# Kernel tuning notes

Measured on AMD Instinct MI355X. Metric: run time of the kernel, lower is better.

Reference implementation:

```python
import jax, jax.numpy as jnp
import numpy as np

D_K = 64
SCALE = D_K ** (-0.5)
B, H, S = 2, 16, 2048


def setup_inputs() -> dict:
    key = jax.random.key(0)
    kq, kk, kv = jax.random.split(key, 3)
    q = jax.random.normal(kq, (B, H, S, D_K), dtype=jnp.float32)
    k = jax.random.normal(kk, (B, H, S, D_K), dtype=jnp.float32)
    v = jax.random.normal(kv, (B, H, S, D_K), dtype=jnp.float32)
    # causal mask: True means masked (matches torch masked_fill semantics)
    mask = jnp.triu(jnp.ones((S, S), dtype=bool), k=1)[None, None]  # [1,1,S,S]
    return {"q": q, "k": k, "v": v, "mask": mask}


def reference(q, k, v, mask) -> jnp.ndarray:
    # scores = q @ k^T  -> [B,H,S,S]
    scores = jnp.einsum("bhqd,bhkd->bhqk", q, k)
    # masked_fill(mask, -inf), then scale (as written in the source),
    # then softmax over the key axis. -inf * scale stays -inf.
    scores = jnp.where(mask, -jnp.inf, scores)
    attn = jax.nn.softmax(SCALE * scores, axis=-1)
    return jnp.einsum("bhqk,bhkd->bhqd", attn, v)
```

## Files before the change

kernel.cpp:

```cpp
#include <hip/hip_runtime.h>
#include <hip/hip_bf16.h>
#include <math.h>


constexpr int S  = 2048;
constexpr int D  = 64;
constexpr int BH = 32;
constexpr float SCALE = 0.125f;
constexpr float LOG2E = 1.4426950408889634f;
constexpr float QPRE  = SCALE * LOG2E;
constexpr int PSTR = 72;

typedef __attribute__((ext_vector_type(8))) short bf16x8;
typedef __attribute__((ext_vector_type(4))) short bf16x4;
typedef __attribute__((ext_vector_type(4))) float f32x4;

#if __has_builtin(__builtin_amdgcn_mfma_f32_16x16x16bf16_1k)
#define HAS_MFMA_1K 1
#else
#define HAS_MFMA_1K 0
#endif

#if __has_builtin(__builtin_amdgcn_exp2f)
#define EXP2F(x) __builtin_amdgcn_exp2f(x)
#else
#define EXP2F(x) exp2f(x)
#endif

__device__ __forceinline__ short f2bf(float x) {
    union { __hip_bfloat16 b; short s; } u; u.b = __float2bfloat16(x); return u.s;
}

__device__ __forceinline__ void gload_lds16(const void* g, void* lds) {
    __builtin_amdgcn_global_load_lds(
        (const __attribute__((address_space(1))) unsigned int*)g,
        (__attribute__((address_space(3))) unsigned int*)lds, 16, 0, 0);
}

__global__ __launch_bounds__(256) void preconv_25993142075924(
    const float* __restrict__ Kg, const float* __restrict__ Vg,
    short* __restrict__ Kb, short* __restrict__ VT)
{
    const int kt = blockIdx.x, bh = blockIdx.y, tid = threadIdx.x;
    __shared__ float lt[64 * 65];
    const float* kp = Kg + (size_t)bh * S * D;
    const float* vp = Vg + (size_t)bh * S * D;
    short* kb = Kb + (size_t)bh * S * D;
    short* vt = VT + (size_t)bh * D * S;
    #pragma unroll
    for (int e = 0; e < 4; ++e) {
        int idx = (tid + e * 256) * 4;
        int r = idx >> 6, c = idx & 63;
        f32x4 k4 = *(const f32x4*)(kp + (size_t)(kt * 64 + r) * D + c);
        bf16x4 kb4;
        kb4[0] = f2bf(k4[0]); kb4[1] = f2bf(k4[1]);
        kb4[2] = f2bf(k4[2]); kb4[3] = f2bf(k4[3]);
        *(bf16x4*)(kb + (size_t)(kt * 64 + r) * D + c) = kb4;
        f32x4 v4 = *(const f32x4*)(vp + (size_t)(kt * 64 + r) * D + c);
        lt[(c + 0) * 65 + r] = v4[0];
        lt[(c + 1) * 65 + r] = v4[1];
        lt[(c + 2) * 65 + r] = v4[2];
        lt[(c + 3) * 65 + r] = v4[3];
    }
    __syncthreads();
    #pragma unroll
    for (int e = 0; e < 2; ++e) {
        int tt = tid + e * 256;
        int d  = tt >> 3;
        int j0 = (tt & 7) * 8;
        bf16x8 o;
        #pragma unroll
        for (int jj = 0; jj < 8; ++jj)
            o[jj] = f2bf(lt[d * 65 + j0 + jj]);
        *(bf16x8*)(vt + (size_t)d * S + kt * 64 + j0) = o;
    }
}

__global__ __launch_bounds__(256, 3) void attn_fwd_v8_25993142075924(
    const float* __restrict__ Qg, const short* __restrict__ Kb,
    const short* __restrict__ VT, float* __restrict__ Og)
{
    const int bh  = blockIdx.x;
    const int qb  = 31 - (int)blockIdx.y;
    const int tid = threadIdx.x;
    const int wv  = tid >> 6;
    const int ln  = tid & 63;
    const int c16 = ln & 15;
    const int qd  = ln >> 4;

    const int q0  = qb * 64 + wv * 16;
    const int nkt = qb + 1;

    __shared__ __align__(16) short lk[2][64 * 64];
    __shared__ __align__(16) short lv[2][64 * 64];
#if !HAS_MFMA_1K
    __shared__ __align__(16) short lp[4 * 16 * PSTR];
    short* lpw = lp + wv * 16 * PSTR;
#endif

    const float* qp = Qg + (size_t)bh * S * D;
    const short* kp = Kb + (size_t)bh * S * D;
    const short* vp = VT + (size_t)bh * D * S;
    float*       op = Og + (size_t)bh * S * D;

    const int srow0 = wv * 16 + (ln >> 3);
    const int sgrp0 = (ln & 7) ^ (srow0 & 7);
    const int srow1 = srow0 + 8;
    const int sgrp1 = (ln & 7) ^ (srow1 & 7);

    bf16x8 qf[2];
    {
        const float* src = qp + (size_t)(q0 + c16) * D + qd * 8;
        #pragma unroll
        for (int khf = 0; khf < 2; ++khf) {
            f32x4 a = *(const f32x4*)(src + khf * 32);
            f32x4 b = *(const f32x4*)(src + khf * 32 + 4);
            bf16x8 f;
            f[0] = f2bf(a[0] * QPRE); f[1] = f2bf(a[1] * QPRE);
            f[2] = f2bf(a[2] * QPRE); f[3] = f2bf(a[3] * QPRE);
            f[4] = f2bf(b[0] * QPRE); f[5] = f2bf(b[1] * QPRE);
            f[6] = f2bf(b[2] * QPRE); f[7] = f2bf(b[3] * QPRE);
            qf[khf] = f;
        }
    }

    f32x4 oacc[4] = {{0,0,0,0},{0,0,0,0},{0,0,0,0},{0,0,0,0}};
    float lsum = 0.f;

    gload_lds16(kp + (size_t)srow0 * D + sgrp0 * 8, &lk[0][(wv * 16 + 0) * 64]);
    gload_lds16(vp + (size_t)srow0 * S + sgrp0 * 8, &lv[0][(wv * 16 + 0) * 64]);
    gload_lds16(kp + (size_t)srow1 * D + sgrp1 * 8, &lk[0][(wv * 16 + 8) * 64]);
    gload_lds16(vp + (size_t)srow1 * S + sgrp1 * 8, &lv[0][(wv * 16 + 8) * 64]);
    __syncthreads();

    for (int kt = 0; kt < nkt; ++kt) {
        const int cur = kt & 1;
        if (kt + 1 < nkt) {
            const int nxt = cur ^ 1;
            const size_t kb0 = (size_t)(kt + 1) * 64;
            gload_lds16(kp + (kb0 + srow0) * D + sgrp0 * 8, &lk[nxt][(wv * 16 + 0) * 64]);
            gload_lds16(vp + (size_t)srow0 * S + kb0 + sgrp0 * 8, &lv[nxt][(wv * 16 + 0) * 64]);
            gload_lds16(kp + (kb0 + srow1) * D + sgrp1 * 8, &lk[nxt][(wv * 16 + 8) * 64]);
            gload_lds16(vp + (size_t)srow1 * S + kb0 + sgrp1 * 8, &lv[nxt][(wv * 16 + 8) * 64]);
        }

#if HAS_MFMA_1K
        bf16x4 vf[4][4];
        #pragma unroll
        for (int dt = 0; dt < 4; ++dt) {
            const int row = dt * 16 + c16;
            #pragma unroll
            for (int nt = 0; nt < 4; ++nt) {
                const int gl = nt * 2 + (qd >> 1);
                const int gp = gl ^ (c16 & 7);
                vf[dt][nt] = *(const bf16x4*)&lv[cur][row * 64 + gp * 8 + (qd & 1) * 4];
            }
        }
#endif

        float t[4][4];
        #pragma unroll
        for (int nt = 0; nt < 4; ++nt) {
            const int row = nt * 16 + c16;
            f32x4 acc = {0,0,0,0};
            #pragma unroll
            for (int khf = 0; khf < 2; ++khf) {
                const int g = (khf * 4 + qd) ^ (row & 7);
                bf16x8 kf = *(const bf16x8*)&lk[cur][row * 64 + g * 8];
                acc = __builtin_amdgcn_mfma_f32_16x16x32_bf16(kf, qf[khf], acc, 0, 0, 0);
            }
            t[nt][0] = acc[0]; t[nt][1] = acc[1]; t[nt][2] = acc[2]; t[nt][3] = acc[3];
        }

        if (kt == qb) {
            #pragma unroll
            for (int nt = 0; nt < 4; ++nt) {
                #pragma unroll
                for (int r = 0; r < 4; ++r) {
                    int key = kt * 64 + nt * 16 + qd * 4 + r;
                    if (key > q0 + c16) t[nt][r] = -INFINITY;
                }
            }
        }

        float pval[4][4];
        #pragma unroll
        for (int nt = 0; nt < 4; ++nt)
            #pragma unroll
            for (int r = 0; r < 4; ++r) {
                float pv = EXP2F(t[nt][r]);
                pval[nt][r] = pv;
                lsum += pv;
            }

#if HAS_MFMA_1K
        #pragma unroll
        for (int nt = 0; nt < 4; ++nt) {
            bf16x4 pf;
            pf[0] = f2bf(pval[nt][0]); pf[1] = f2bf(pval[nt][1]);
            pf[2] = f2bf(pval[nt][2]); pf[3] = f2bf(pval[nt][3]);
            #pragma unroll
            for (int dt = 0; dt < 4; ++dt)
                oacc[dt] = __builtin_amdgcn_mfma_f32_16x16x16bf16_1k(
                    vf[dt][nt], pf, oacc[dt], 0, 0, 0);
        }
#else
        #pragma unroll
        for (int nt = 0; nt < 4; ++nt)
            #pragma unroll
            for (int r = 0; r < 4; ++r)
                lpw[c16 * PSTR + nt * 16 + qd * 4 + r] = f2bf(pval[nt][r]);
        bf16x8 pf2[2];
        #pragma unroll
        for (int khf = 0; khf < 2; ++khf)
            pf2[khf] = *(const bf16x8*)&lpw[c16 * PSTR + khf * 32 + qd * 8];
        #pragma unroll
        for (int dt = 0; dt < 4; ++dt) {
            const int row = dt * 16 + c16;
            #pragma unroll
            for (int khf = 0; khf < 2; ++khf) {
                const int g = (khf * 4 + qd) ^ (row & 7);
                bf16x8 vf8 = *(const bf16x8*)&lv[cur][row * 64 + g * 8];
                oacc[dt] = __builtin_amdgcn_mfma_f32_16x16x32_bf16(vf8, pf2[khf], oacc[dt], 0, 0, 0);
            }
        }
#endif

        __syncthreads();
    }

    float s = lsum;
    s += __shfl_xor(s, 16);
    s += __shfl_xor(s, 32);
    const float inv = 1.0f / s;
    float* dst = op + (size_t)(q0 + c16) * D;
    #pragma unroll
    for (int dt = 0; dt < 4; ++dt) {
        f32x4 o;
        o[0] = oacc[dt][0] * inv; o[1] = oacc[dt][1] * inv;
        o[2] = oacc[dt][2] * inv; o[3] = oacc[dt][3] * inv;
        *(f32x4*)(dst + dt * 16 + qd * 4) = o;
    }
}

__global__ __launch_bounds__(256) void attn_fwd_v1_25993142075924(
    const float* __restrict__ Qg, const float* __restrict__ Kg,
    const float* __restrict__ Vg, float* __restrict__ Og)
{
    constexpr int KSTR = 72;
    constexpr int BQ = 64, BK = 64;
    const int qt  = blockIdx.x;
    const int bh  = blockIdx.y;
    const int tid = threadIdx.x;
    const int wv  = tid >> 6;
    const int ln  = tid & 63;
    const int c16 = ln & 15;
    const int qd  = ln >> 4;

    __shared__ __align__(16) __hip_bfloat16 lk [BK][KSTR];
    __shared__ __align__(16) __hip_bfloat16 lvt[D ][KSTR];
    __shared__ __align__(16) __hip_bfloat16 lp [4][16][KSTR];

    const size_t hoff = (size_t)bh * S * D;
    const float* qp = Qg + hoff;
    const float* kp = Kg + hoff;
    const float* vp = Vg + hoff;
    float*       op = Og + hoff;
    const int q0 = qt * BQ;

    bf16x8 qf[2];
    {
        const float* src = qp + (size_t)(q0 + wv*16 + c16) * D + qd*8;
        #pragma unroll
        for (int kh = 0; kh < 2; ++kh) {
            f32x4 a = *(const f32x4*)(src + kh*32);
            f32x4 b = *(const f32x4*)(src + kh*32 + 4);
            bf16x8 f;
            f[0]=f2bf(a[0]*QPRE); f[1]=f2bf(a[1]*QPRE); f[2]=f2bf(a[2]*QPRE); f[3]=f2bf(a[3]*QPRE);
            f[4]=f2bf(b[0]*QPRE); f[5]=f2bf(b[1]*QPRE); f[6]=f2bf(b[2]*QPRE); f[7]=f2bf(b[3]*QPRE);
            qf[kh] = f;
        }
    }

    f32x4 oacc[4] = {{0,0,0,0},{0,0,0,0},{0,0,0,0},{0,0,0,0}};
    float mrun[4] = {-INFINITY,-INFINITY,-INFINITY,-INFINITY};
    float lrun[4] = {0.f,0.f,0.f,0.f};

    const int nkt = qt + 1;
    for (int kt = 0; kt < nkt; ++kt) {
        __syncthreads();
        #pragma unroll
        for (int e = 0; e < 4; ++e) {
            int idx = (tid + e*256) * 4;
            int row = idx >> 6, col = idx & 63;
            f32x4 k4 = *(const f32x4*)(kp + (size_t)(kt*BK + row)*D + col);
            bf16x4 kb;
            kb[0]=f2bf(k4[0]); kb[1]=f2bf(k4[1]); kb[2]=f2bf(k4[2]); kb[3]=f2bf(k4[3]);
            *(bf16x4*)&lk[row][col] = kb;
            f32x4 v4 = *(const f32x4*)(vp + (size_t)(kt*BK + row)*D + col);
            lvt[col+0][row] = __float2bfloat16(v4[0]);
            lvt[col+1][row] = __float2bfloat16(v4[1]);
            lvt[col+2][row] = __float2bfloat16(v4[2]);
            lvt[col+3][row] = __float2bfloat16(v4[3]);
        }
        __syncthreads();

        float t[4][4];
        #pragma unroll
        for (int nt = 0; nt < 4; ++nt) {
            f32x4 acc = {0,0,0,0};
            #pragma unroll
            for (int kh = 0; kh < 2; ++kh) {
                bf16x8 kf = *(const bf16x8*)&lk[nt*16 + c16][kh*32 + qd*8];
                acc = __builtin_amdgcn_mfma_f32_16x16x32_bf16(qf[kh], kf, acc, 0, 0, 0);
            }
            #pragma unroll
            for (int r = 0; r < 4; ++r) t[nt][r] = acc[r];
        }
        if (kt == nkt - 1) {
            #pragma unroll
            for (int nt = 0; nt < 4; ++nt) {
                int j = kt*BK + nt*16 + c16;
                #pragma unroll
                for (int r = 0; r < 4; ++r)
                    if (j > q0 + wv*16 + qd*4 + r) t[nt][r] = -INFINITY;
            }
        }

        float pval[4][4];
        #pragma unroll
        for (int r = 0; r < 4; ++r) {
            float tm = fmaxf(fmaxf(t[0][r], t[1][r]), fmaxf(t[2][r], t[3][r]));
            tm = fmaxf(tm, __shfl_xor(tm, 1));
            tm = fmaxf(tm, __shfl_xor(tm, 2));
            tm = fmaxf(tm, __shfl_xor(tm, 4));
            tm = fmaxf(tm, __shfl_xor(tm, 8));
            float mnew  = fmaxf(mrun[r], tm);
            float alpha = exp2f(mrun[r] - mnew);
            mrun[r] = mnew;
            float rs = 0.f;
            #pragma unroll
            for (int nt = 0; nt < 4; ++nt) {
                float pv = exp2f(t[nt][r] - mnew);
                pval[nt][r] = pv;
                rs += pv;
            }
            rs += __shfl_xor(rs, 1);
            rs += __shfl_xor(rs, 2);
            rs += __shfl_xor(rs, 4);
            rs += __shfl_xor(rs, 8);
            lrun[r] = lrun[r] * alpha + rs;
            #pragma unroll
            for (int dt = 0; dt < 4; ++dt) oacc[dt][r] *= alpha;
        }

        #pragma unroll
        for (int nt = 0; nt < 4; ++nt)
            #pragma unroll
            for (int r = 0; r < 4; ++r)
                lp[wv][qd*4 + r][nt*16 + c16] = __float2bfloat16(pval[nt][r]);
        bf16x8 pf[2];
        #pragma unroll
        for (int kh = 0; kh < 2; ++kh)
            pf[kh] = *(const bf16x8*)&lp[wv][c16][kh*32 + qd*8];

        #pragma unroll
        for (int dt = 0; dt < 4; ++dt) {
            #pragma unroll
            for (int kh = 0; kh < 2; ++kh) {
                bf16x8 vf = *(const bf16x8*)&lvt[dt*16 + c16][kh*32 + qd*8];
                oacc[dt] = __builtin_amdgcn_mfma_f32_16x16x32_bf16(pf[kh], vf, oacc[dt], 0, 0, 0);
            }
        }
    }

    #pragma unroll
    for (int r = 0; r < 4; ++r) {
        float inv = 1.0f / lrun[r];
        float* dst = op + (size_t)(q0 + wv*16 + qd*4 + r) * D;
        #pragma unroll
        for (int dt = 0; dt < 4; ++dt)
            dst[dt*16 + c16] = oacc[dt][r] * inv;
    }
}

extern "C" void kernel_launch(void* const* d_in, const int* in_sizes, int n_in,
                              void* d_out, int out_size, void* d_ws, size_t ws_size,
                              hipStream_t stream) {
    const float* q = (const float*)d_in[0];
    const float* k = (const float*)d_in[1];
    const float* v = (const float*)d_in[2];
    float* out = (float*)d_out;
    const size_t elems = (size_t)BH * S * D;
    const size_t need  = 2 * elems * sizeof(short);
    if (ws_size >= need) {
        short* Kb = (short*)d_ws;
        short* VT = Kb + elems;
        preconv_25993142075924<<<dim3(S / 64, BH), 256, 0, stream>>>(k, v, Kb, VT);
        attn_fwd_v8_25993142075924<<<dim3(BH, 32), 256, 0, stream>>>(q, Kb, VT, out);
    } else {
        attn_fwd_v1_25993142075924<<<dim3(S / 64, BH), 256, 0, stream>>>(q, k, v, out);
    }
}
```

Baseline: 137.1 us.

## Process 128 query rows per block, reusing K/V tiles across two query sub-tiles

Each block now covers 128 query rows instead of 64, and each wave handles two 16-row query sub-tiles. Every K and V tile loaded into LDS therefore feeds twice the MFMA work, which halves the global-to-LDS traffic per query. Waves skip compute on tiles that lie fully above their causal diagonal. The launch bound drops to 2 blocks per SM, the grid halves to 16 q-blocks per head ordered in a zig-zag to balance causal work, and register pressure rises. Some waves idle on diagonal tiles.

```diff
diff --git a/kernel.cpp b/kernel.cpp
--- a/kernel.cpp
+++ b/kernel.cpp
@@ -76,20 +76,22 @@
     }
 }
 
-__global__ __launch_bounds__(256, 3) void attn_fwd_v8_25993142075924(
+__global__ __launch_bounds__(256, 2) void attn_fwd_v9_25993142075924(
     const float* __restrict__ Qg, const short* __restrict__ Kb,
     const short* __restrict__ VT, float* __restrict__ Og)
 {
     const int bh  = blockIdx.x;
-    const int qb  = 31 - (int)blockIdx.y;
+    const int yy  = blockIdx.y;
+    const int qb  = (yy < 8) ? (15 - yy) : (yy - 8);
     const int tid = threadIdx.x;
     const int wv  = tid >> 6;
     const int ln  = tid & 63;
     const int c16 = ln & 15;
     const int qd  = ln >> 4;
 
-    const int q0  = qb * 64 + wv * 16;
-    const int nkt = qb + 1;
+    const int w0    = qb * 128 + wv * 32;
+    const int nkt   = 2 * qb + 2;
+    const int mask0 = w0 >> 6;
 
     __shared__ __align__(16) short lk[2][64 * 64];
     __shared__ __align__(16) short lv[2][64 * 64];
@@ -108,9 +110,10 @@
     const int srow1 = srow0 + 8;
     const int sgrp1 = (ln & 7) ^ (srow1 & 7);
 
-    bf16x8 qf[2];
-    {
-        const float* src = qp + (size_t)(q0 + c16) * D + qd * 8;
+    bf16x8 qf[2][2];
+    #pragma unroll
+    for (int sp = 0; sp < 2; ++sp) {
+        const float* src = qp + (size_t)(w0 + sp * 16 + c16) * D + qd * 8;
         #pragma unroll
         for (int khf = 0; khf < 2; ++khf) {
             f32x4 a = *(const f32x4*)(src + khf * 32);
@@ -120,12 +123,13 @@
             f[2] = f2bf(a[2] * QPRE); f[3] = f2bf(a[3] * QPRE);
             f[4] = f2bf(b[0] * QPRE); f[5] = f2bf(b[1] * QPRE);
             f[6] = f2bf(b[2] * QPRE); f[7] = f2bf(b[3] * QPRE);
-            qf[khf] = f;
-        }
-    }
-
-    f32x4 oacc[4] = {{0,0,0,0},{0,0,0,0},{0,0,0,0},{0,0,0,0}};
-    float lsum = 0.f;
+            qf[sp][khf] = f;
+        }
+    }
+
+    f32x4 oacc[2][4] = {{{0,0,0,0},{0,0,0,0},{0,0,0,0},{0,0,0,0}},
+                        {{0,0,0,0},{0,0,0,0},{0,0,0,0},{0,0,0,0}}};
+    float lsum[2] = {0.f, 0.f};
 
     gload_lds16(kp + (size_t)srow0 * D + sgrp0 * 8, &lk[0][(wv * 16 + 0) * 64]);
     gload_lds16(vp + (size_t)srow0 * S + sgrp0 * 8, &lv[0][(wv * 16 + 0) * 64]);
@@ -144,102 +148,112 @@
             gload_lds16(vp + (size_t)srow1 * S + kb0 + sgrp1 * 8, &lv[nxt][(wv * 16 + 8) * 64]);
         }
 
+        if (kt * 64 <= w0 + 31) {
 #if HAS_MFMA_1K
-        bf16x4 vf[4][4];
+            bf16x4 vf[4][4];
+            #pragma unroll
+            for (int dt = 0; dt < 4; ++dt) {
+                const int row = dt * 16 + c16;
+                #pragma unroll
+                for (int nt = 0; nt < 4; ++nt) {
+                    const int gl = nt * 2 + (qd >> 1);
+                    const int gp = gl ^ (c16 & 7);
+                    vf[dt][nt] = *(const bf16x4*)&lv[cur][row * 64 + gp * 8 + (qd & 1) * 4];
+                }
+            }
+#endif
+
+            float t0[4][4], t1[4][4];
+            #pragma unroll
+            for (int nt = 0; nt < 4; ++nt) {
+                const int row = nt * 16 + c16;
+                f32x4 a0 = {0,0,0,0}, a1 = {0,0,0,0};
+                #pragma unroll
+                for (int khf = 0; khf < 2; ++khf) {
+                    const int g = (khf * 4 + qd) ^ (row & 7);
+                    bf16x8 kf = *(const bf16x8*)&lk[cur][row * 64 + g * 8];
+                    a0 = __builtin_amdgcn_mfma_f32_16x16x32_bf16(kf, qf[0][khf], a0, 0, 0, 0);
+                    a1 = __builtin_amdgcn_mfma_f32_16x16x32_bf16(kf, qf[1][khf], a1, 0, 0, 0);
+                }
+                #pragma unroll
+                for (int r = 0; r < 4; ++r) { t0[nt][r] = a0[r]; t1[nt][r] = a1[r]; }
+            }
+
+            if (kt >= mask0) {
+                #pragma unroll
+                for (int nt = 0; nt < 4; ++nt) {
+                    #pragma unroll
+                    for (int r = 0; r < 4; ++r) {
+                        int key = kt * 64 + nt * 16 + qd * 4 + r;
+                        if (key > w0 + c16)      t0[nt][r] = -INFINITY;
+                        if (key > w0 + 16 + c16) t1[nt][r] = -INFINITY;
+                    }
+                }
+            }
+
+            #pragma unroll
+            for (int sp = 0; sp < 2; ++sp) {
+                float (&t)[4][4] = sp ? t1 : t0;
+#if HAS_MFMA_1K
+                #pragma unroll
+                for (int nt = 0; nt < 4; ++nt) {
+                    bf16x4 pf;
+                    #pragma unroll
+                    for (int r = 0; r < 4; ++r) {
+                        float pv = EXP2F(t[nt][r]);
+                        lsum[sp] += pv;
+                        pf[r] = f2bf(pv);
+                    }
+                    #pragma unroll
+                    for (int dt = 0; dt < 4; ++dt)
+                        oacc[sp][dt] = __builtin_amdgcn_mfma_f32_16x16x16bf16_1k(
+                            vf[dt][nt], pf, oacc[sp][dt], 0, 0, 0);
+                }
+#else
+                #pragma unroll
+                for (int nt = 0; nt < 4; ++nt)
+                    #pragma unroll
+                    for (int r = 0; r < 4; ++r) {
+                        float pv = EXP2F(t[nt][r]);
+                        lsum[sp] += pv;
+                        lpw[c16 * PSTR + nt * 16 + qd * 4 + r] = f2bf(pv);
+                    }
+                bf16x8 pf2[2];
+                #pragma unroll
+                for (int khf = 0; khf < 2; ++khf)
+                    pf2[khf] = *(const bf16x8*)&lpw[c16 * PSTR + khf * 32 + qd * 8];
+                #pragma unroll
+                for (int dt = 0; dt < 4; ++dt) {
+                    const int row = dt * 16 + c16;
+                    #pragma unroll
+                    for (int khf = 0; khf < 2; ++khf) {
+                        const int g = (khf * 4 + qd) ^ (row & 7);
+                        bf16x8 vf8 = *(const bf16x8*)&lv[cur][row * 64 + g * 8];
+                        oacc[sp][dt] = __builtin_amdgcn_mfma_f32_16x16x32_bf16(
+                            vf8, pf2[khf], oacc[sp][dt], 0, 0, 0);
+                    }
+                }
+#endif
+            }
+        }
+
+        __syncthreads();
+    }
+
+    #pragma unroll
+    for (int sp = 0; sp < 2; ++sp) {
+        float s2 = lsum[sp];
+        s2 += __shfl_xor(s2, 16);
+        s2 += __shfl_xor(s2, 32);
+        const float inv = 1.0f / s2;
+        float* dst = op + (size_t)(w0 + sp * 16 + c16) * D;
         #pragma unroll
         for (int dt = 0; dt < 4; ++dt) {
-            const int row = dt * 16 + c16;
-            #pragma unroll
-            for (int nt = 0; nt < 4; ++nt) {
-                const int gl = nt * 2 + (qd >> 1);
-                const int gp = gl ^ (c16 & 7);
-                vf[dt][nt] = *(const bf16x4*)&lv[cur][row * 64 + gp * 8 + (qd & 1) * 4];
-            }
-        }
-#endif
-
-        float t[4][4];
-        #pragma unroll
-        for (int nt = 0; nt < 4; ++nt) {
-            const int row = nt * 16 + c16;
-            f32x4 acc = {0,0,0,0};
-            #pragma unroll
-            for (int khf = 0; khf < 2; ++khf) {
-                const int g = (khf * 4 + qd) ^ (row & 7);
-                bf16x8 kf = *(const bf16x8*)&lk[cur][row * 64 + g * 8];
-                acc = __builtin_amdgcn_mfma_f32_16x16x32_bf16(kf, qf[khf], acc, 0, 0, 0);
-            }
-            t[nt][0] = acc[0]; t[nt][1] = acc[1]; t[nt][2] = acc[2]; t[nt][3] = acc[3];
-        }
-
-        if (kt == qb) {
-            #pragma unroll
-            for (int nt = 0; nt < 4; ++nt) {
-                #pragma unroll
-                for (int r = 0; r < 4; ++r) {
-                    int key = kt * 64 + nt * 16 + qd * 4 + r;
-                    if (key > q0 + c16) t[nt][r] = -INFINITY;
-                }
-            }
-        }
-
-        float pval[4][4];
-        #pragma unroll
-        for (int nt = 0; nt < 4; ++nt)
-            #pragma unroll
-            for (int r = 0; r < 4; ++r) {
-                float pv = EXP2F(t[nt][r]);
-                pval[nt][r] = pv;
-                lsum += pv;
-            }
-
-#if HAS_MFMA_1K
-        #pragma unroll
-        for (int nt = 0; nt < 4; ++nt) {
-            bf16x4 pf;
-            pf[0] = f2bf(pval[nt][0]); pf[1] = f2bf(pval[nt][1]);
-            pf[2] = f2bf(pval[nt][2]); pf[3] = f2bf(pval[nt][3]);
-            #pragma unroll
-            for (int dt = 0; dt < 4; ++dt)
-                oacc[dt] = __builtin_amdgcn_mfma_f32_16x16x16bf16_1k(
-                    vf[dt][nt], pf, oacc[dt], 0, 0, 0);
-        }
-#else
-        #pragma unroll
-        for (int nt = 0; nt < 4; ++nt)
-            #pragma unroll
-            for (int r = 0; r < 4; ++r)
-                lpw[c16 * PSTR + nt * 16 + qd * 4 + r] = f2bf(pval[nt][r]);
-        bf16x8 pf2[2];
-        #pragma unroll
-        for (int khf = 0; khf < 2; ++khf)
-            pf2[khf] = *(const bf16x8*)&lpw[c16 * PSTR + khf * 32 + qd * 8];
-        #pragma unroll
-        for (int dt = 0; dt < 4; ++dt) {
-            const int row = dt * 16 + c16;
-            #pragma unroll
-            for (int khf = 0; khf < 2; ++khf) {
-                const int g = (khf * 4 + qd) ^ (row & 7);
-                bf16x8 vf8 = *(const bf16x8*)&lv[cur][row * 64 + g * 8];
-                oacc[dt] = __builtin_amdgcn_mfma_f32_16x16x32_bf16(vf8, pf2[khf], oacc[dt], 0, 0, 0);
-            }
-        }
-#endif
-
-        __syncthreads();
-    }
-
-    float s = lsum;
-    s += __shfl_xor(s, 16);
-    s += __shfl_xor(s, 32);
-    const float inv = 1.0f / s;
-    float* dst = op + (size_t)(q0 + c16) * D;
-    #pragma unroll
-    for (int dt = 0; dt < 4; ++dt) {
-        f32x4 o;
-        o[0] = oacc[dt][0] * inv; o[1] = oacc[dt][1] * inv;
-        o[2] = oacc[dt][2] * inv; o[3] = oacc[dt][3] * inv;
-        *(f32x4*)(dst + dt * 16 + qd * 4) = o;
+            f32x4 o;
+            o[0] = oacc[sp][dt][0] * inv; o[1] = oacc[sp][dt][1] * inv;
+            o[2] = oacc[sp][dt][2] * inv; o[3] = oacc[sp][dt][3] * inv;
+            *(f32x4*)(dst + dt * 16 + qd * 4) = o;
+        }
     }
 }
 
@@ -397,7 +411,7 @@
         short* Kb = (short*)d_ws;
         short* VT = Kb + elems;
         preconv_25993142075924<<<dim3(S / 64, BH), 256, 0, stream>>>(k, v, Kb, VT);
-        attn_fwd_v8_25993142075924<<<dim3(BH, 32), 256, 0, stream>>>(q, Kb, VT, out);
+        attn_fwd_v9_25993142075924<<<dim3(BH, 16), 256, 0, stream>>>(q, Kb, VT, out);
     } else {
         attn_fwd_v1_25993142075924<<<dim3(S / 64, BH), 256, 0, stream>>>(q, k, v, out);
     }
```

After: 142.1 us. 3.6% more time.

## Triple-buffer K tiles with staggered K/V prefetch and explicit vmcnt barriers

Applied to the files above, without the earlier changes.

K tiles move to a three-deep LDS ring and are prefetched two iterations ahead, while V stays double-buffered and is prefetched one ahead. The full __syncthreads is replaced by a partial s_waitcnt vmcnt plus s_barrier, so later loads can stay in flight across iterations. MFMA sections are wrapped in s_setprio, and the launch bound rises to 4 blocks per CU. The aim is to hide global-to-LDS latency. The cost is more LDS per block and tight vmcnt accounting that must match the number of loads issued.

```diff
diff --git a/kernel.cpp b/kernel.cpp
--- a/kernel.cpp
+++ b/kernel.cpp
@@ -76,7 +76,7 @@
     }
 }
 
-__global__ __launch_bounds__(256, 3) void attn_fwd_v8_25993142075924(
+__global__ __launch_bounds__(256, 4) void attn_fwd_v10_25993142075924(
     const float* __restrict__ Qg, const short* __restrict__ Kb,
     const short* __restrict__ VT, float* __restrict__ Og)
 {
@@ -91,7 +91,7 @@
     const int q0  = qb * 64 + wv * 16;
     const int nkt = qb + 1;
 
-    __shared__ __align__(16) short lk[2][64 * 64];
+    __shared__ __align__(16) short lk[3][64 * 64];
     __shared__ __align__(16) short lv[2][64 * 64];
 #if !HAS_MFMA_1K
     __shared__ __align__(16) short lp[4 * 16 * PSTR];
@@ -127,22 +127,36 @@
     f32x4 oacc[4] = {{0,0,0,0},{0,0,0,0},{0,0,0,0},{0,0,0,0}};
     float lsum = 0.f;
 
-    gload_lds16(kp + (size_t)srow0 * D + sgrp0 * 8, &lk[0][(wv * 16 + 0) * 64]);
-    gload_lds16(vp + (size_t)srow0 * S + sgrp0 * 8, &lv[0][(wv * 16 + 0) * 64]);
-    gload_lds16(kp + (size_t)srow1 * D + sgrp1 * 8, &lk[0][(wv * 16 + 8) * 64]);
-    gload_lds16(vp + (size_t)srow1 * S + sgrp1 * 8, &lv[0][(wv * 16 + 8) * 64]);
-    __syncthreads();
-
+    #define STAGE_K(t, b)                                                          \
+        do {                                                                       \
+            gload_lds16(kp + ((size_t)(t) * 64 + srow0) * D + sgrp0 * 8,           \
+                        &lk[b][(wv * 16 + 0) * 64]);                               \
+            gload_lds16(kp + ((size_t)(t) * 64 + srow1) * D + sgrp1 * 8,           \
+                        &lk[b][(wv * 16 + 8) * 64]);                               \
+        } while (0)
+    #define STAGE_V(t, b)                                                          \
+        do {                                                                       \
+            gload_lds16(vp + (size_t)srow0 * S + (t) * 64 + sgrp0 * 8,             \
+                        &lv[b][(wv * 16 + 0) * 64]);                               \
+            gload_lds16(vp + (size_t)srow1 * S + (t) * 64 + sgrp1 * 8,             \
+                        &lv[b][(wv * 16 + 8) * 64]);                               \
+        } while (0)
+
+    STAGE_K(0, 0);
+    STAGE_V(0, 0);
+    if (nkt > 1) {
+        STAGE_K(1, 1);
+        asm volatile("s_waitcnt vmcnt(2)" ::: "memory");
+    } else {
+        asm volatile("s_waitcnt vmcnt(0)" ::: "memory");
+    }
+    __builtin_amdgcn_s_barrier();
+
+    int kcur = 0, kst = 2;
     for (int kt = 0; kt < nkt; ++kt) {
-        const int cur = kt & 1;
-        if (kt + 1 < nkt) {
-            const int nxt = cur ^ 1;
-            const size_t kb0 = (size_t)(kt + 1) * 64;
-            gload_lds16(kp + (kb0 + srow0) * D + sgrp0 * 8, &lk[nxt][(wv * 16 + 0) * 64]);
-            gload_lds16(vp + (size_t)srow0 * S + kb0 + sgrp0 * 8, &lv[nxt][(wv * 16 + 0) * 64]);
-            gload_lds16(kp + (kb0 + srow1) * D + sgrp1 * 8, &lk[nxt][(wv * 16 + 8) * 64]);
-            gload_lds16(vp + (size_t)srow1 * S + kb0 + sgrp1 * 8, &lv[nxt][(wv * 16 + 8) * 64]);
-        }
+        const int vcur = kt & 1;
+        if (kt + 1 < nkt) STAGE_V(kt + 1, vcur ^ 1);
+        if (kt + 2 < nkt) STAGE_K(kt + 2, kst);
 
 #if HAS_MFMA_1K
         bf16x4 vf[4][4];
@@ -153,12 +167,13 @@
             for (int nt = 0; nt < 4; ++nt) {
                 const int gl = nt * 2 + (qd >> 1);
                 const int gp = gl ^ (c16 & 7);
-                vf[dt][nt] = *(const bf16x4*)&lv[cur][row * 64 + gp * 8 + (qd & 1) * 4];
+                vf[dt][nt] = *(const bf16x4*)&lv[vcur][row * 64 + gp * 8 + (qd & 1) * 4];
             }
         }
 #endif
 
         float t[4][4];
+        __builtin_amdgcn_s_setprio(1);
         #pragma unroll
         for (int nt = 0; nt < 4; ++nt) {
             const int row = nt * 16 + c16;
@@ -166,11 +181,12 @@
             #pragma unroll
             for (int khf = 0; khf < 2; ++khf) {
                 const int g = (khf * 4 + qd) ^ (row & 7);
-                bf16x8 kf = *(const bf16x8*)&lk[cur][row * 64 + g * 8];
+                bf16x8 kf = *(const bf16x8*)&lk[kcur][row * 64 + g * 8];
                 acc = __builtin_amdgcn_mfma_f32_16x16x32_bf16(kf, qf[khf], acc, 0, 0, 0);
             }
             t[nt][0] = acc[0]; t[nt][1] = acc[1]; t[nt][2] = acc[2]; t[nt][3] = acc[3];
         }
+        __builtin_amdgcn_s_setprio(0);
 
         if (kt == qb) {
             #pragma unroll
@@ -194,6 +210,7 @@
             }
 
 #if HAS_MFMA_1K
+        __builtin_amdgcn_s_setprio(1);
         #pragma unroll
         for (int nt = 0; nt < 4; ++nt) {
             bf16x4 pf;
@@ -204,6 +221,7 @@
                 oacc[dt] = __builtin_amdgcn_mfma_f32_16x16x16bf16_1k(
                     vf[dt][nt], pf, oacc[dt], 0, 0, 0);
         }
+        __builtin_amdgcn_s_setprio(0);
 #else
         #pragma unroll
         for (int nt = 0; nt < 4; ++nt)
@@ -220,14 +238,24 @@
             #pragma unroll
             for (int khf = 0; khf < 2; ++khf) {
                 const int g = (khf * 4 + qd) ^ (row & 7);
-                bf16x8 vf8 = *(const bf16x8*)&lv[cur][row * 64 + g * 8];
+                bf16x8 vf8 = *(const bf16x8*)&lv[vcur][row * 64 + g * 8];
                 oacc[dt] = __builtin_amdgcn_mfma_f32_16x16x32_bf16(vf8, pf2[khf], oacc[dt], 0, 0, 0);
             }
         }
 #endif
 
-        __syncthreads();
-    }
+        if (kt + 2 < nkt) {
+            asm volatile("s_waitcnt vmcnt(2)" ::: "memory");
+            __builtin_amdgcn_s_barrier();
+        } else if (kt + 1 < nkt) {
+            asm volatile("s_waitcnt vmcnt(0)" ::: "memory");
+            __builtin_amdgcn_s_barrier();
+        }
+        kcur = (kcur == 2) ? 0 : kcur + 1;
+        kst  = (kst  == 2) ? 0 : kst  + 1;
+    }
+    #undef STAGE_K
+    #undef STAGE_V
 
     float s = lsum;
     s += __shfl_xor(s, 16);
@@ -397,7 +425,7 @@
         short* Kb = (short*)d_ws;
         short* VT = Kb + elems;
         preconv_25993142075924<<<dim3(S / 64, BH), 256, 0, stream>>>(k, v, Kb, VT);
-        attn_fwd_v8_25993142075924<<<dim3(BH, 32), 256, 0, stream>>>(q, Kb, VT, out);
+        attn_fwd_v10_25993142075924<<<dim3(BH, 32), 256, 0, stream>>>(q, Kb, VT, out);
     } else {
         attn_fwd_v1_25993142075924<<<dim3(S / 64, BH), 256, 0, stream>>>(q, k, v, out);
     }
```

Result: slower. 141.9 us (+3.5%).
